# Kernel tuning notes

Hardware: AMD Instinct MI355X
Metric: run time of the kernel (lower is better)

The kernel has to match this reference:

```python
import jax, jax.numpy as jnp
import numpy as np

WINDOW_SIZE = 11
SIGMA = 1.5
C1 = 0.01 ** 2
C2 = 0.03 ** 2


def _gaussian_window(channel, window_size=WINDOW_SIZE, sigma=SIGMA):
    # Faithful to the torch code: the 1D gaussian is NOT normalized.
    x = jnp.arange(window_size, dtype=jnp.float32)
    g = jnp.exp(-((x - window_size // 2) ** 2) / (2.0 * sigma ** 2))
    w2d = jnp.outer(g, g)  # [ws, ws]
    return jnp.broadcast_to(w2d[None, None], (channel, 1, window_size, window_size))


def _dwconv(x, window, window_size, channel):
    # depthwise conv2d with SAME-ish padding = window_size // 2
    pad = window_size // 2
    return jax.lax.conv_general_dilated(
        x, window,
        window_strides=(1, 1),
        padding=[(pad, pad), (pad, pad)],
        dimension_numbers=("NCHW", "OIHW", "NCHW"),
        feature_group_count=channel,
    )


def setup_inputs() -> dict:
    key = jax.random.key(0)
    k1, k2 = jax.random.split(key)
    B, C, H, W = 16, 3, 512, 512
    img1 = jax.random.uniform(k1, (B, C, H, W), dtype=jnp.float32)
    img2 = jax.random.uniform(k2, (B, C, H, W), dtype=jnp.float32)
    return {"img1": img1, "img2": img2}


def reference(img1, img2):
    channel = img1.shape[1]
    window = _gaussian_window(channel).astype(img1.dtype)

    mu1 = _dwconv(img1, window, WINDOW_SIZE, channel)
    mu2 = _dwconv(img2, window, WINDOW_SIZE, channel)
    mu1_sq = mu1 * mu1
    mu2_sq = mu2 * mu2
    mu1_mu2 = mu1 * mu2

    sigma1_sq = _dwconv(img1 * img1, window, WINDOW_SIZE, channel) - mu1_sq
    sigma2_sq = _dwconv(img2 * img2, window, WINDOW_SIZE, channel) - mu2_sq
    sigma12 = _dwconv(img1 * img2, window, WINDOW_SIZE, channel) - mu1_mu2

    ssim_map = ((2.0 * mu1_mu2 + C1) * (2.0 * sigma12 + C2)) / (
        (mu1_sq + mu2_sq + C1) * (sigma1_sq + sigma2_sq + C2)
    )
    # size_average=True -> scalar mean
    return 1.0 - jnp.mean(ssim_map)
```

## Files before the change

### kernel.cpp

```cpp
#include <hip/hip_runtime.h>


typedef float v2f __attribute__((ext_vector_type(2)));

#define IMG   512
#define NIMG  48
#define TW    32
#define TH    32
#define PH    42
#define SSTR  46
#define HSTR  46
#define TILES 16
#define NBLOCKS (NIMG * TILES * TILES)

#define G0 0.0038659204f
#define G1 0.0285655010f
#define G2 0.1353352832f
#define G3 0.4111123050f
#define G4 0.8007374029f
#define G5 1.0f

__global__ __launch_bounds__(256, 4) void ssim_tile_kernel(
    const float* __restrict__ img1, const float* __restrict__ img2,
    float* __restrict__ partials)
{
    __shared__ v2f ssd[PH][SSTR];
    __shared__ v2f sh2[2][TW][HSTR];
    __shared__ float s_part[4];

    const float gw[11] = {G0,G1,G2,G3,G4,G5,G4,G3,G2,G1,G0};

    const int tid = threadIdx.x;
    const int tx0 = blockIdx.x * TW - 5;
    const int ty0 = blockIdx.y * TH - 5;
    const float* __restrict__ p1 = img1 + (size_t)blockIdx.z * (IMG * IMG);
    const float* __restrict__ p2 = img2 + (size_t)blockIdx.z * (IMG * IMG);

    {
        const bool interior = (blockIdx.x >= 1) && (blockIdx.x <= TILES - 2) &&
                              (blockIdx.y >= 1) && (blockIdx.y <= TILES - 2);
        int r = tid / 42;
        int c = tid - r * 42;
        if (interior) {
#pragma unroll
            for (int it = 0; it < 7; ++it) {
                if (it < 6 || r < PH) {
                    int gi = (ty0 + r) * IMG + (tx0 + c);
                    float a = p1[gi], b = p2[gi];
                    ssd[r][c] = (v2f){a + b, a - b};
                }
                c += 4; r += 6;
                if (c >= 42) { c -= 42; r += 1; }
            }
        } else {
#pragma unroll
            for (int it = 0; it < 7; ++it) {
                if (it < 6 || r < PH) {
                    int gr = ty0 + r, gc = tx0 + c;
                    bool ok = ((unsigned)gr < IMG) && ((unsigned)gc < IMG);
                    int gi = gr * IMG + gc;
                    float a = ok ? p1[gi] : 0.0f;
                    float b = ok ? p2[gi] : 0.0f;
                    ssd[r][c] = (v2f){a + b, a - b};
                }
                c += 4; r += 6;
                if (c >= 42) { c -= 42; r += 1; }
            }
        }
    }

    const bool hact = tid < 168;
    const int  hr  = hact ? (tid % 42) : 0;
    const int  hc0 = hact ? ((tid / 42) * 8) : 0;

    const int col = tid & 31;
    const int r0  = (tid >> 5) * 4;

    __syncthreads();

    if (hact) {
        v2f v[20];
        {
            const float4* src = (const float4*)&ssd[hr][hc0];
#pragma unroll
            for (int q = 0; q < 10; ++q) ((float4*)v)[q] = src[q];
        }
        v2f m[8];
#pragma unroll
        for (int j = 0; j < 8; ++j) m[j] = (v2f){0.f, 0.f};
#pragma unroll
        for (int k = 0; k < 11; ++k) {
            const v2f wv = {gw[k], gw[k]};
#pragma unroll
            for (int j = 0; j < 8; ++j)
                m[j] = __builtin_elementwise_fma(v[j + k], wv, m[j]);
        }
#pragma unroll
        for (int j = 0; j < 8; ++j) sh2[0][hc0 + j][hr] = m[j];
#pragma unroll
        for (int e = 0; e < 18; ++e) v[e] *= v[e];
        v2f x[8];
#pragma unroll
        for (int j = 0; j < 8; ++j) x[j] = (v2f){0.f, 0.f};
#pragma unroll
        for (int k = 0; k < 11; ++k) {
            const v2f wv = {gw[k], gw[k]};
#pragma unroll
            for (int j = 0; j < 8; ++j)
                x[j] = __builtin_elementwise_fma(v[j + k], wv, x[j]);
        }
#pragma unroll
        for (int j = 0; j < 8; ++j) sh2[1][hc0 + j][hr] = x[j];
    }
    __syncthreads();

    v2f am[4], ax[4];
    {
        v2f hb[16];
        {
            const float4* s0 = (const float4*)&sh2[0][col][r0];
#pragma unroll
            for (int q = 0; q < 8; ++q) ((float4*)hb)[q] = s0[q];
        }
#pragma unroll
        for (int i = 0; i < 4; ++i) {
            v2f s = {0.f, 0.f};
#pragma unroll
            for (int k = 0; k < 11; ++k) {
                const v2f wv = {gw[k], gw[k]};
                s = __builtin_elementwise_fma(wv, hb[i + k], s);
            }
            am[i] = s;
        }
        {
            const float4* s1 = (const float4*)&sh2[1][col][r0];
#pragma unroll
            for (int q = 0; q < 8; ++q) ((float4*)hb)[q] = s1[q];
        }
#pragma unroll
        for (int i = 0; i < 4; ++i) {
            v2f s = {0.f, 0.f};
#pragma unroll
            for (int k = 0; k < 11; ++k) {
                const v2f wv = {gw[k], gw[k]};
                s = __builtin_elementwise_fma(wv, hb[i + k], s);
            }
            ax[i] = s;
        }
    }

    const float C1 = 1.0e-4f, C2 = 9.0e-4f;
    float local = 0.f;
#pragma unroll
    for (int i = 0; i < 4; ++i) {
        v2f mu = am[i];
        v2f mu2 = mu * mu;
        float sum2 = 0.5f  * (mu2[0] + mu2[1]);
        float m12  = 0.25f * (mu2[0] - mu2[1]);
        v2f xx = ax[i];
        float xsum = 0.5f  * (xx[0] + xx[1]);
        float x12  = 0.25f * (xx[0] - xx[1]);
        float sg12  = x12 - m12;
        float sgsum = xsum - sum2;
        float num = (2.f * m12 + C1) * (2.f * sg12 + C2);
        float den = (sum2 + C1) * (sgsum + C2);
        local = fmaf(num, __builtin_amdgcn_rcpf(den), local);
    }

#pragma unroll
    for (int off = 32; off > 0; off >>= 1)
        local += __shfl_down(local, off, 64);
    if ((tid & 63) == 0) s_part[tid >> 6] = local;
    __syncthreads();
    if (tid == 0) {
        int bidx = (blockIdx.z * gridDim.y + blockIdx.y) * gridDim.x + blockIdx.x;
        partials[bidx] = s_part[0] + s_part[1] + s_part[2] + s_part[3];
    }
}

__global__ __launch_bounds__(256) void ssim_final_kernel(
    const float* __restrict__ partials, float* __restrict__ out)
{
    __shared__ double sp[4];
    double acc = 0.0;
    for (int i = threadIdx.x; i < NBLOCKS; i += 256)
        acc += (double)partials[i];
#pragma unroll
    for (int off = 32; off > 0; off >>= 1)
        acc += __shfl_down(acc, off, 64);
    if ((threadIdx.x & 63) == 0) sp[threadIdx.x >> 6] = acc;
    __syncthreads();
    if (threadIdx.x == 0) {
        double total = sp[0] + sp[1] + sp[2] + sp[3];
        out[0] = (float)(1.0 - total / (double)((size_t)NIMG * IMG * IMG));
    }
}

extern "C" void kernel_launch(void* const* d_in, const int* in_sizes, int n_in,
                              void* d_out, int out_size, void* d_ws, size_t ws_size,
                              hipStream_t stream) {
    const float* img1 = (const float*)d_in[0];
    const float* img2 = (const float*)d_in[1];
    float* out = (float*)d_out;
    float* partials = (float*)d_ws;

    dim3 grid(TILES, TILES, NIMG);
    ssim_tile_kernel<<<grid, dim3(256), 0, stream>>>(img1, img2, partials);
    ssim_final_kernel<<<1, dim3(256), 0, stream>>>(partials, out);
}
```

Before: 169.3 us.

## Load horizontal-pass inputs straight from global memory, dropping staging LDS tile

Removes the shared-memory staging tile and one barrier. Each horizontal-pass thread now reads its 20-wide row segment directly from global memory using unaligned float4 loads and builds the sum/difference pairs in registers. Launch bounds occupancy hint is raised from 4 to 6 blocks per CU, which the smaller LDS footprint allows. In exchange, global reads overlap between threads (each pixel is loaded about 2.5 times and relies on cache), the float4 loads are unaligned, and the 88 threads that only work in the vertical pass no longer help with loading.

```diff
diff --git a/kernel.cpp b/kernel.cpp
--- a/kernel.cpp
+++ b/kernel.cpp
@@ -2,13 +2,13 @@
 
 
 typedef float v2f __attribute__((ext_vector_type(2)));
+typedef float float4u __attribute__((ext_vector_type(4), aligned(4)));
 
 #define IMG   512
 #define NIMG  48
 #define TW    32
 #define TH    32
 #define PH    42
-#define SSTR  46
 #define HSTR  46
 #define TILES 16
 #define NBLOCKS (NIMG * TILES * TILES)
@@ -20,11 +20,10 @@
 #define G4 0.8007374029f
 #define G5 1.0f
 
-__global__ __launch_bounds__(256, 4) void ssim_tile_kernel(
+__global__ __launch_bounds__(256, 6) void ssim_tile_kernel(
     const float* __restrict__ img1, const float* __restrict__ img2,
     float* __restrict__ partials)
 {
-    __shared__ v2f ssd[PH][SSTR];
     __shared__ v2f sh2[2][TW][HSTR];
     __shared__ float s_part[4];
 
@@ -36,54 +35,41 @@
     const float* __restrict__ p1 = img1 + (size_t)blockIdx.z * (IMG * IMG);
     const float* __restrict__ p2 = img2 + (size_t)blockIdx.z * (IMG * IMG);
 
-    {
-        const bool interior = (blockIdx.x >= 1) && (blockIdx.x <= TILES - 2) &&
-                              (blockIdx.y >= 1) && (blockIdx.y <= TILES - 2);
-        int r = tid / 42;
-        int c = tid - r * 42;
-        if (interior) {
-#pragma unroll
-            for (int it = 0; it < 7; ++it) {
-                if (it < 6 || r < PH) {
-                    int gi = (ty0 + r) * IMG + (tx0 + c);
-                    float a = p1[gi], b = p2[gi];
-                    ssd[r][c] = (v2f){a + b, a - b};
-                }
-                c += 4; r += 6;
-                if (c >= 42) { c -= 42; r += 1; }
-            }
-        } else {
-#pragma unroll
-            for (int it = 0; it < 7; ++it) {
-                if (it < 6 || r < PH) {
-                    int gr = ty0 + r, gc = tx0 + c;
-                    bool ok = ((unsigned)gr < IMG) && ((unsigned)gc < IMG);
-                    int gi = gr * IMG + gc;
-                    float a = ok ? p1[gi] : 0.0f;
-                    float b = ok ? p2[gi] : 0.0f;
-                    ssd[r][c] = (v2f){a + b, a - b};
-                }
-                c += 4; r += 6;
-                if (c >= 42) { c -= 42; r += 1; }
-            }
-        }
-    }
-
     const bool hact = tid < 168;
     const int  hr  = hact ? (tid % 42) : 0;
     const int  hc0 = hact ? ((tid / 42) * 8) : 0;
 
-    const int col = tid & 31;
-    const int r0  = (tid >> 5) * 4;
-
-    __syncthreads();
-
     if (hact) {
         v2f v[20];
         {
-            const float4* src = (const float4*)&ssd[hr][hc0];
+            const int gr  = ty0 + hr;
+            const int gc0 = tx0 + hc0;
+            const bool interior = (blockIdx.x >= 1) && (blockIdx.x <= TILES - 2) &&
+                                  (blockIdx.y >= 1) && (blockIdx.y <= TILES - 2);
+            if (interior) {
+                const float* r1 = p1 + gr * IMG + gc0;
+                const float* r2 = p2 + gr * IMG + gc0;
 #pragma unroll
-            for (int q = 0; q < 10; ++q) ((float4*)v)[q] = src[q];
+                for (int q = 0; q < 5; ++q) {
+                    float4u A = *(const float4u*)&r1[4 * q];
+                    float4u B = *(const float4u*)&r2[4 * q];
+#pragma unroll
+                    for (int j = 0; j < 4; ++j)
+                        v[4 * q + j] = (v2f){A[j] + B[j], A[j] - B[j]};
+                }
+            } else {
+                const bool rok = (unsigned)gr < IMG;
+                const float* r1 = p1 + gr * IMG;
+                const float* r2 = p2 + gr * IMG;
+#pragma unroll
+                for (int e = 0; e < 20; ++e) {
+                    int gc = gc0 + e;
+                    bool ok = rok && ((unsigned)gc < IMG);
+                    float a = ok ? r1[gc] : 0.0f;
+                    float b = ok ? r2[gc] : 0.0f;
+                    v[e] = (v2f){a + b, a - b};
+                }
+            }
         }
         v2f m[8];
 #pragma unroll
@@ -114,6 +100,8 @@
     }
     __syncthreads();
 
+    const int col = tid & 31;
+    const int r0  = (tid >> 5) * 4;
     v2f am[4], ax[4];
     {
         v2f hb[16];
```

Measured after the change: 231.0 us. 36.5% more time.
